# Kernel tuning notes

Hardware: AMD Instinct MI355X
Metric: run time of the kernel (lower is better)

Reference implementation:

```python
import jax, jax.numpy as jnp
import numpy as np

HEADS = 8
NUM_LANDMARKS = 256
PINV_ITERS = 6
KERNEL = 33
PAD = KERNEL // 2


def moore_penrose_iter_pinv(x, iters=PINV_ITERS):
    abs_x = jnp.abs(x)
    col = abs_x.sum(axis=-1)
    row = abs_x.sum(axis=-2)
    z = jnp.swapaxes(x, -1, -2) / (jnp.max(col) * jnp.max(row))
    I = jnp.eye(x.shape[-1], dtype=x.dtype)
    for _ in range(iters):
        xz = x @ z
        z = 0.25 * z @ (13.0 * I - xz @ (15.0 * I - xz @ (7.0 * I - xz)))
    return z


def setup_inputs() -> dict:
    key = jax.random.key(0)
    k1, k2, k3, k4 = jax.random.split(key, 4)
    b, h, n, d = 2, HEADS, 8192, 64
    q = jax.random.normal(k1, (b, h, n, d), dtype=jnp.float32)
    k = jax.random.normal(k2, (b, h, n, d), dtype=jnp.float32)
    v = jax.random.normal(k3, (b, h, n, d), dtype=jnp.float32)
    conv_w = jax.random.normal(k4, (HEADS, 1, KERNEL, 1), dtype=jnp.float32) * 0.05
    return {"q": q, "k": k, "v": v, "conv_w": conv_w}


def reference(q, k, v, conv_w):
    b, h, n, d = q.shape
    m = NUM_LANDMARKS
    l = n // m  # n chosen divisible by m, so no padding branch

    # landmarks: mean over contiguous groups of size l
    q_land = q.reshape(b, h, m, l, d).sum(axis=-2) / l  # [b,h,m,d]
    k_land = k.reshape(b, h, m, l, d).sum(axis=-2) / l

    sim1 = jnp.einsum('bhid,bhjd->bhij', q, k_land)       # [b,h,n,m]
    sim2 = jnp.einsum('bhid,bhjd->bhij', q_land, k_land)  # [b,h,m,m]
    sim3 = jnp.einsum('bhid,bhjd->bhij', q_land, k)       # [b,h,m,n]

    attn1 = jax.nn.softmax(sim1, axis=-1)
    attn2 = jax.nn.softmax(sim2, axis=-1)
    attn3 = jax.nn.softmax(sim3, axis=-1)

    attn2_inv = moore_penrose_iter_pinv(attn2, PINV_ITERS)

    out = attn1 @ (attn2_inv @ (attn3 @ v))  # [b,h,n,d]

    # depthwise residual conv over sequence dim (Conv2d(h,h,(33,1),groups=h,bias=False) on v)
    res = jax.lax.conv_general_dilated(
        v, conv_w,
        window_strides=(1, 1),
        padding=((PAD, PAD), (0, 0)),
        dimension_numbers=('NCHW', 'OIHW', 'NCHW'),
        feature_group_count=HEADS,
    )
    return out + res
```

## Files before the change

### kernel.cpp

```cpp
#include <hip/hip_runtime.h>


#define N_SEQ 8192
#define NBH   16
#define MLAND 256
#define DHEAD 64
#define NSPLIT3 8
#define MM_E  (NBH * MLAND * MLAND)
#define LM_E  (NBH * MLAND * DHEAD)

typedef __attribute__((ext_vector_type(8))) short bfrag;
typedef __attribute__((ext_vector_type(8))) _Float16 hfrag;
typedef __attribute__((ext_vector_type(4))) float f32x4;

__device__ __forceinline__ void fma8(float (&o)[8], float p, const float4& a, const float4& b) {
    o[0] += p * a.x; o[1] += p * a.y; o[2] += p * a.z; o[3] += p * a.w;
    o[4] += p * b.x; o[5] += p * b.y; o[6] += p * b.z; o[7] += p * b.w;
}

__device__ __forceinline__ float bf2f(unsigned short h) {
    return __uint_as_float(((unsigned)h) << 16);
}

__device__ __forceinline__ void splitbf(float v, unsigned short& h, unsigned short& l) {
    unsigned bits = __float_as_uint(v);
    h = (unsigned short)(bits >> 16);
    float r = v - __uint_as_float(bits & 0xffff0000u);
    l = (unsigned short)(__float_as_uint(r) >> 16);
}

__device__ __forceinline__ void splith(float v, unsigned short& h, unsigned short& l) {
    _Float16 hf = (_Float16)v;
    _Float16 lf = (_Float16)(v - (float)hf);
    h = __builtin_bit_cast(unsigned short, hf);
    l = __builtin_bit_cast(unsigned short, lf);
}

__device__ __forceinline__ void stage16(const float* __restrict__ src,
                                        unsigned short* dh, unsigned short* dl) {
    unsigned* ph = (unsigned*)dh;
    unsigned* pl = (unsigned*)dl;
    #pragma unroll
    for (int o = 0; o < 16; o += 4) {
        float4 a = *(const float4*)(src + o);
        float vv[4] = {a.x, a.y, a.z, a.w};
        unsigned short h[4], l[4];
        #pragma unroll
        for (int u = 0; u < 4; ++u) splitbf(vv[u], h[u], l[u]);
        ph[o / 2]     = (unsigned)h[0] | ((unsigned)h[1] << 16);
        ph[o / 2 + 1] = (unsigned)h[2] | ((unsigned)h[3] << 16);
        pl[o / 2]     = (unsigned)l[0] | ((unsigned)l[1] << 16);
        pl[o / 2 + 1] = (unsigned)l[2] | ((unsigned)l[3] << 16);
    }
}

__device__ __forceinline__ void stageh16(const float* __restrict__ src,
                                         unsigned short* dh, unsigned short* dl) {
    unsigned* ph = (unsigned*)dh;
    unsigned* pl = (unsigned*)dl;
    #pragma unroll
    for (int o = 0; o < 16; o += 4) {
        float4 a = *(const float4*)(src + o);
        float vv[4] = {a.x, a.y, a.z, a.w};
        unsigned short h[4], l[4];
        #pragma unroll
        for (int u = 0; u < 4; ++u) splith(vv[u], h[u], l[u]);
        ph[o / 2]     = (unsigned)h[0] | ((unsigned)h[1] << 16);
        ph[o / 2 + 1] = (unsigned)h[2] | ((unsigned)h[3] << 16);
        pl[o / 2]     = (unsigned)l[0] | ((unsigned)l[1] << 16);
        pl[o / 2 + 1] = (unsigned)l[2] | ((unsigned)l[3] << 16);
    }
}

__global__ __launch_bounds__(64) void k_landmarks(
    const float* __restrict__ q, const float* __restrict__ k,
    float* __restrict__ ql, float* __restrict__ kl)
{
    int mi = blockIdx.x & 255;
    int bh = blockIdx.x >> 8;
    const float* src = blockIdx.y ? k : q;
    float*       dst = blockIdx.y ? kl : ql;
    int t = threadIdx.x;
    const float* s = src + ((size_t)bh * N_SEQ + (size_t)mi * 32) * DHEAD;
    float acc = 0.f;
    #pragma unroll
    for (int j = 0; j < 32; ++j) acc += s[j * DHEAD + t];
    dst[((size_t)bh * MLAND + mi) * DHEAD + t] = acc * (1.f / 32.f);
}

__global__ __launch_bounds__(256) void k_sim2_softmax(
    const float* __restrict__ ql, const float* __restrict__ kl,
    unsigned short* __restrict__ xs)
{
    unsigned short* xh = xs;
    unsigned short* xl = xs + MM_E;
    int bh = blockIdx.x >> 8;
    int i  = blockIdx.x & 255;
    int t  = threadIdx.x;
    __shared__ float qrow[DHEAD];
    __shared__ float wred[8];
    if (t < DHEAD) qrow[t] = ql[((size_t)bh * MLAND + i) * DHEAD + t];
    __syncthreads();
    const float* krow = kl + ((size_t)bh * MLAND + t) * DHEAD;
    float s = 0.f;
    #pragma unroll
    for (int kk = 0; kk < DHEAD; kk += 4) {
        float4 k4 = *(const float4*)(krow + kk);
        s += qrow[kk] * k4.x + qrow[kk + 1] * k4.y + qrow[kk + 2] * k4.z + qrow[kk + 3] * k4.w;
    }
    float m = s;
    #pragma unroll
    for (int o = 32; o > 0; o >>= 1) m = fmaxf(m, __shfl_xor(m, o, 64));
    int wave = t >> 6, lane = t & 63;
    if (lane == 0) wred[wave] = m;
    __syncthreads();
    float bm = fmaxf(fmaxf(wred[0], wred[1]), fmaxf(wred[2], wred[3]));
    float e = __expf(s - bm);
    float sum = e;
    #pragma unroll
    for (int o = 32; o > 0; o >>= 1) sum += __shfl_xor(sum, o, 64);
    if (lane == 0) wred[4 + wave] = sum;
    __syncthreads();
    float bs = wred[4] + wred[5] + wred[6] + wred[7];
    float val = e / bs;
    unsigned short h, l;
    splitbf(val, h, l);
    size_t idx = ((size_t)bh * MLAND + i) * MLAND + t;
    xh[idx] = h;
    xl[idx] = l;
}

__global__ __launch_bounds__(256) void k_scale_reduce(
    const unsigned short* __restrict__ xs, float* __restrict__ scl)
{
    const unsigned short* xh = xs;
    const unsigned short* xl = xs + MM_E;
    int bh = blockIdx.x, t = threadIdx.x;
    size_t b = (size_t)bh * MLAND * MLAND;
    float colsum = 0.f, rowsum = 0.f;
    for (int i = 0; i < MLAND; ++i) {
        size_t idx = b + (size_t)i * MLAND + t;
        colsum += bf2f(xh[idx]) + bf2f(xl[idx]);
    }
    for (int j = 0; j < MLAND; ++j) {
        size_t idx = b + (size_t)t * MLAND + j;
        rowsum += bf2f(xh[idx]) + bf2f(xl[idx]);
    }
    __shared__ float red[256];
    red[t] = rowsum;
    __syncthreads();
    for (int o = 128; o > 0; o >>= 1) {
        if (t < o) red[t] = fmaxf(red[t], red[t + o]);
        __syncthreads();
    }
    if (t == 0) atomicMax((unsigned int*)&scl[0], __float_as_uint(red[0]));
    __syncthreads();
    red[t] = colsum;
    __syncthreads();
    for (int o = 128; o > 0; o >>= 1) {
        if (t < o) red[t] = fmaxf(red[t], red[t + o]);
        __syncthreads();
    }
    if (t == 0) atomicMax((unsigned int*)&scl[1], __float_as_uint(red[0]));
}

__global__ __launch_bounds__(256) void k_zinit(
    const unsigned short* __restrict__ xs, unsigned short* __restrict__ zs,
    const float* __restrict__ scl)
{
    const unsigned short* xh = xs;
    const unsigned short* xl = xs + MM_E;
    unsigned short* zh = zs;
    unsigned short* zl = zs + MM_E;
    __shared__ float tile[32][33];
    int bh = blockIdx.z;
    int i0 = blockIdx.y * 32, j0 = blockIdx.x * 32;
    int t = threadIdx.x;
    int lx = t & 31, ly = t >> 5;
    size_t b = (size_t)bh * MLAND * MLAND;
    #pragma unroll
    for (int p = 0; p < 4; ++p) {
        size_t idx = b + (size_t)(i0 + ly + 8 * p) * MLAND + j0 + lx;
        tile[ly + 8 * p][lx] = bf2f(xh[idx]) + bf2f(xl[idx]);
    }
    __syncthreads();
    float inv = 1.0f / (scl[0] * scl[1]);
    #pragma unroll
    for (int p = 0; p < 4; ++p) {
        float val = tile[lx][ly + 8 * p] * inv;
        unsigned short h, l;
        splitbf(val, h, l);
        size_t idx = b + (size_t)(j0 + ly + 8 * p) * MLAND + i0 + lx;
        zh[idx] = h;
        zl[idx] = l;
    }
}

__global__ __launch_bounds__(256) void k_bmm_planes(
    const unsigned short* __restrict__ Ahp, const unsigned short* __restrict__ Alp,
    const unsigned short* __restrict__ Bhp, const unsigned short* __restrict__ Blp,
    unsigned short* __restrict__ Chp, unsigned short* __restrict__ Clp,
    float* __restrict__ Cf,
    int N, float diag, float bscale, float outscale)
{
    __shared__ unsigned short sm[2 * 32 * 72 + 2 * 64 * 72];
    unsigned short* Ah = sm;
    unsigned short* Al = sm + 32 * 72;
    unsigned short* Bh = sm + 2 * 32 * 72;
    unsigned short* Bl = sm + 2 * 32 * 72 + 64 * 72;

    int bh = blockIdx.z;
    const size_t abase = (size_t)bh * 65536;
    const size_t bbase = (size_t)bh * 256 * N;
    int m0 = blockIdx.y * 32, n0 = blockIdx.x * 64;
    int t = threadIdx.x;
    int wave = t >> 6, lane = t & 63;
    int l15 = lane & 15, quad = lane >> 4;
    int wr = wave >> 1, wc = wave & 1;
    unsigned sflip = (bscale < 0.f) ? 0x8000u : 0u;

    f32x4 acc[2] = {};

    for (int kc = 0; kc < 256; kc += 64) {
        __syncthreads();
        {
            int m = t & 31, ks = (t >> 5) * 8;
            size_t off = abase + (size_t)(m0 + m) * 256 + kc + ks;
            *(uint4*)&Ah[m * 72 + ks] = *(const uint4*)&Ahp[off];
            *(uint4*)&Al[m * 72 + ks] = *(const uint4*)&Alp[off];
        }
        {
            int kk = t & 63, ns = (t >> 6) * 16;
            int gk = kc + kk;
            size_t off = bbase + (size_t)gk * N + n0 + ns;
            unsigned short hb[16], lb[16];
            *(uint4*)&hb[0] = *(const uint4*)&Bhp[off];
            *(uint4*)&hb[8] = *(const uint4*)&Bhp[off + 8];
            *(uint4*)&lb[0] = *(const uint4*)&Blp[off];
            *(uint4*)&lb[8] = *(const uint4*)&Blp[off + 8];
            #pragma unroll
            for (int u = 0; u < 16; ++u) {
                unsigned short h = hb[u] ^ sflip;
                unsigned short l = lb[u] ^ sflip;
                if (diag != 0.f && gk == n0 + ns + u) {
                    float val = diag + bf2f(h) + bf2f(l);
                    splitbf(val, h, l);
                }
                Bh[(ns + u) * 72 + kk] = h;
                Bl[(ns + u) * 72 + kk] = l;
            }
        }
        __syncthreads();

        #pragma unroll
        for (int k0 = 0; k0 < 64; k0 += 32) {
            int kf = k0 + quad * 8;
            int am = wr * 16 + l15;
            bfrag ah = *(const bfrag*)&Ah[am * 72 + kf];
            bfrag al = *(const bfrag*)&Al[am * 72 + kf];
            #pragma unroll
            for (int j = 0; j < 2; ++j) {
                int bn = wc * 32 + j * 16 + l15;
                bfrag bhf = *(const bfrag*)&Bh[bn * 72 + kf];
                bfrag blf = *(const bfrag*)&Bl[bn * 72 + kf];
                acc[j] = __builtin_amdgcn_mfma_f32_16x16x32_bf16(al, bhf, acc[j], 0, 0, 0);
                acc[j] = __builtin_amdgcn_mfma_f32_16x16x32_bf16(ah, blf, acc[j], 0, 0, 0);
                acc[j] = __builtin_amdgcn_mfma_f32_16x16x32_bf16(ah, bhf, acc[j], 0, 0, 0);
            }
        }
    }

    size_t cbase = (size_t)bh * 256 * N;
    if (Cf) {
        #pragma unroll
        for (int j = 0; j < 2; ++j) {
            #pragma unroll
            for (int r = 0; r < 4; ++r) {
                int row = m0 + wr * 16 + quad * 4 + r;
                int col = n0 + wc * 32 + j * 16 + l15;
                Cf[cbase + (size_t)row * N + col] = acc[j][r] * outscale;
            }
        }
    } else {
        #pragma unroll
        for (int j = 0; j < 2; ++j) {
            #pragma unroll
            for (int r = 0; r < 4; ++r) {
                int row = m0 + wr * 16 + quad * 4 + r;
                int col = n0 + wc * 32 + j * 16 + l15;
                float val = acc[j][r] * outscale;
                unsigned short h, l;
                splitbf(val, h, l);
                size_t idx = cbase + (size_t)row * N + col;
                Chp[idx] = h;
                Clp[idx] = l;
            }
        }
    }
}

__global__ __launch_bounds__(256, 2) void k_attn3_partial(
    const float* __restrict__ ql, const float* __restrict__ k,
    const float* __restrict__ v, float* __restrict__ pO,
    float* __restrict__ pm, float* __restrict__ pl)
{
    __shared__ __align__(16) unsigned short sm3[36864];
    unsigned short* QH = sm3;
    unsigned short* QL = sm3 + 4608;
    unsigned short* KH = sm3 + 9216;
    unsigned short* KL = sm3 + 13824;
    unsigned short* VH = sm3 + 18432;
    unsigned short* VL = sm3 + 23040;
    unsigned short* PH = sm3 + 27648;
    unsigned short* PL = sm3 + 32256;

    int sp = blockIdx.x;
    int m0 = blockIdx.y * 64;
    int bh = blockIdx.z;
    int t = threadIdx.x;
    int wave = t >> 6, lane = t & 63;
    int l15 = lane & 15, quad = lane >> 4;

    {
        int row = t & 63, ds = (t >> 6) * 16;
        const float* src = ql + ((size_t)bh * MLAND + m0 + row) * DHEAD + ds;
        stage16(src, &QH[row * 72 + ds], &QL[row * 72 + ds]);
    }
    __syncthreads();

    bfrag aqh[2], aql[2];
    #pragma unroll
    for (int ks = 0; ks < 2; ++ks) {
        aqh[ks] = *(const bfrag*)&QH[(wave * 16 + l15) * 72 + ks * 32 + quad * 8];
        aql[ks] = *(const bfrag*)&QL[(wave * 16 + l15) * 72 + ks * 32 + quad * 8];
    }

    f32x4 O[4] = {};
    float M[4], L[4];
    #pragma unroll
    for (int r = 0; r < 4; ++r) { M[r] = -1e30f; L[r] = 0.f; }

    const float* kb = k + (size_t)bh * N_SEQ * DHEAD;
    const float* vb = v + (size_t)bh * N_SEQ * DHEAD;

    for (int cc = 0; cc < 16; ++cc) {
        int c0 = sp * 1024 + cc * 64;
        __syncthreads();
        {
            int key = t & 63, ds = (t >> 6) * 16;
            stage16(kb + (size_t)(c0 + key) * DHEAD + ds,
                    &KH[key * 72 + ds], &KL[key * 72 + ds]);
        }
        {
            int key = t & 63, dq = (t >> 6) * 16;
            const float* src = vb + (size_t)(c0 + key) * DHEAD + dq;
            #pragma unroll
            for (int o = 0; o < 16; o += 4) {
                float4 a = *(const float4*)(src + o);
                float vv[4] = {a.x, a.y, a.z, a.w};
                #pragma unroll
                for (int u = 0; u < 4; ++u) {
                    unsigned short h, l;
                    splitbf(vv[u], h, l);
                    VH[(dq + o + u) * 72 + key] = h;
                    VL[(dq + o + u) * 72 + key] = l;
                }
            }
        }
        __syncthreads();

        f32x4 S4[4] = {};
        __builtin_amdgcn_s_setprio(1);
        #pragma unroll
        for (int ks = 0; ks < 2; ++ks) {
            #pragma unroll
            for (int ni = 0; ni < 4; ++ni) {
                bfrag bkh = *(const bfrag*)&KH[(ni * 16 + l15) * 72 + ks * 32 + quad * 8];
                bfrag bkl = *(const bfrag*)&KL[(ni * 16 + l15) * 72 + ks * 32 + quad * 8];
                S4[ni] = __builtin_amdgcn_mfma_f32_16x16x32_bf16(aql[ks], bkh, S4[ni], 0, 0, 0);
                S4[ni] = __builtin_amdgcn_mfma_f32_16x16x32_bf16(aqh[ks], bkl, S4[ni], 0, 0, 0);
                S4[ni] = __builtin_amdgcn_mfma_f32_16x16x32_bf16(aqh[ks], bkh, S4[ni], 0, 0, 0);
            }
        }
        __builtin_amdgcn_s_setprio(0);

        #pragma unroll
        for (int r = 0; r < 4; ++r) {
            float mv = fmaxf(fmaxf(S4[0][r], S4[1][r]), fmaxf(S4[2][r], S4[3][r]));
            mv = fmaxf(mv, __shfl_xor(mv, 1, 16));
            mv = fmaxf(mv, __shfl_xor(mv, 2, 16));
            mv = fmaxf(mv, __shfl_xor(mv, 4, 16));
            mv = fmaxf(mv, __shfl_xor(mv, 8, 16));
            float nM = fmaxf(M[r], mv);
            float alpha = __expf(M[r] - nM);
            M[r] = nM;
            float rs = 0.f;
            #pragma unroll
            for (int ni = 0; ni < 4; ++ni) {
                float p = __expf(S4[ni][r] - nM);
                S4[ni][r] = p;
                rs += p;
            }
            rs += __shfl_xor(rs, 1, 16);
            rs += __shfl_xor(rs, 2, 16);
            rs += __shfl_xor(rs, 4, 16);
            rs += __shfl_xor(rs, 8, 16);
            L[r] = L[r] * alpha + rs;
            #pragma unroll
            for (int ni = 0; ni < 4; ++ni) O[ni][r] *= alpha;
        }

        #pragma unroll
        for (int ni = 0; ni < 4; ++ni) {
            #pragma unroll
            for (int r = 0; r < 4; ++r) {
                int row = wave * 16 + quad * 4 + r;
                int col = ni * 16 + l15;
                unsigned short h, l;
                splitbf(S4[ni][r], h, l);
                PH[row * 72 + col] = h;
                PL[row * 72 + col] = l;
            }
        }

        __builtin_amdgcn_s_setprio(1);
        #pragma unroll
        for (int ks = 0; ks < 2; ++ks) {
            bfrag aph = *(const bfrag*)&PH[(wave * 16 + l15) * 72 + ks * 32 + quad * 8];
            bfrag apl = *(const bfrag*)&PL[(wave * 16 + l15) * 72 + ks * 32 + quad * 8];
            #pragma unroll
            for (int ni = 0; ni < 4; ++ni) {
                bfrag bvh = *(const bfrag*)&VH[(ni * 16 + l15) * 72 + ks * 32 + quad * 8];
                bfrag bvl = *(const bfrag*)&VL[(ni * 16 + l15) * 72 + ks * 32 + quad * 8];
                O[ni] = __builtin_amdgcn_mfma_f32_16x16x32_bf16(apl, bvh, O[ni], 0, 0, 0);
                O[ni] = __builtin_amdgcn_mfma_f32_16x16x32_bf16(aph, bvl, O[ni], 0, 0, 0);
                O[ni] = __builtin_amdgcn_mfma_f32_16x16x32_bf16(aph, bvh, O[ni], 0, 0, 0);
            }
        }
        __builtin_amdgcn_s_setprio(0);
    }

    int base = (bh * NSPLIT3 + sp) * MLAND + m0;
    #pragma unroll
    for (int r = 0; r < 4; ++r) {
        int row = wave * 16 + quad * 4 + r;
        if (l15 == 0) { pm[base + row] = M[r]; pl[base + row] = L[r]; }
        #pragma unroll
        for (int ni = 0; ni < 4; ++ni)
            pO[(size_t)(base + row) * DHEAD + ni * 16 + l15] = O[ni][r];
    }
}

__global__ __launch_bounds__(64) void k_attn3_combine(
    const float* __restrict__ pO, const float* __restrict__ pm,
    const float* __restrict__ pl, unsigned short* __restrict__ kvs)
{
    unsigned short* kvh = kvs;
    unsigned short* kvl = kvs + LM_E;
    int bh = blockIdx.x >> 8;
    int m  = blockIdx.x & 255;
    int d  = threadIdx.x;
    float M = -1e30f;
    #pragma unroll
    for (int s = 0; s < NSPLIT3; ++s) M = fmaxf(M, pm[(bh * NSPLIT3 + s) * MLAND + m]);
    float L = 0.f, O = 0.f;
    #pragma unroll
    for (int s = 0; s < NSPLIT3; ++s) {
        int base = (bh * NSPLIT3 + s) * MLAND + m;
        float w = __expf(pm[base] - M);
        L += pl[base] * w;
        O += w * pO[(size_t)base * DHEAD + d];
    }
    float val = O / L;
    unsigned short h, l;
    splitbf(val, h, l);
    size_t idx = ((size_t)bh * MLAND + m) * DHEAD + d;
    kvh[idx] = h;
    kvl[idx] = l;
}

__global__ __launch_bounds__(256, 2) void k_attn1_mfma(
    const float* __restrict__ q, const float* __restrict__ kl,
    const float* __restrict__ W, float* __restrict__ out)
{
    __shared__ __align__(16) unsigned short sm1[36864];
    unsigned short* QH = sm1;
    unsigned short* QL = sm1 + 4608;
    unsigned short* KH = sm1 + 9216;
    unsigned short* KL = sm1 + 13824;
    unsigned short* WH = sm1 + 18432;
    unsigned short* WL = sm1 + 23040;
    unsigned short* PH = sm1 + 27648;
    unsigned short* PL = sm1 + 32256;

    int bh = blockIdx.y;
    int r0 = blockIdx.x * 64;
    int t = threadIdx.x;
    int wave = t >> 6, lane = t & 63;
    int l15 = lane & 15, quad = lane >> 4;

    {
        int row = t & 63, ds = (t >> 6) * 16;
        const float* src = q + ((size_t)bh * N_SEQ + r0 + row) * DHEAD + ds;
        stageh16(src, &QH[row * 72 + ds], &QL[row * 72 + ds]);
    }
    __syncthreads();

    hfrag aqh[2], aql[2];
    #pragma unroll
    for (int ks = 0; ks < 2; ++ks) {
        aqh[ks] = *(const hfrag*)&QH[(wave * 16 + l15) * 72 + ks * 32 + quad * 8];
        aql[ks] = *(const hfrag*)&QL[(wave * 16 + l15) * 72 + ks * 32 + quad * 8];
    }

    f32x4 O4[4] = {};
    float M[4], L[4];
    #pragma unroll
    for (int r = 0; r < 4; ++r) { M[r] = -1e30f; L[r] = 0.f; }

    for (int mc = 0; mc < 4; ++mc) {
        __syncthreads();
        {
            int key = t & 63, ds = (t >> 6) * 16;
            stageh16(kl + ((size_t)bh * MLAND + mc * 64 + key) * DHEAD + ds,
                     &KH[key * 72 + ds], &KL[key * 72 + ds]);
        }
        {
            int key = t & 63, dq = (t >> 6) * 16;
            const float* src = W + ((size_t)bh * MLAND + mc * 64 + key) * DHEAD + dq;
            #pragma unroll
            for (int o = 0; o < 16; o += 4) {
                float4 a = *(const float4*)(src + o);
                float vv[4] = {a.x * 0.015625f, a.y * 0.015625f,
                               a.z * 0.015625f, a.w * 0.015625f};
                #pragma unroll
                for (int u = 0; u < 4; ++u) {
                    unsigned short h, l;
                    splith(vv[u], h, l);
                    WH[(dq + o + u) * 72 + key] = h;
                    WL[(dq + o + u) * 72 + key] = l;
                }
            }
        }
        __syncthreads();

        f32x4 S4[4] = {};
        __builtin_amdgcn_s_setprio(1);
        #pragma unroll
        for (int ks = 0; ks < 2; ++ks) {
            #pragma unroll
            for (int ni = 0; ni < 4; ++ni) {
                hfrag bkh = *(const hfrag*)&KH[(ni * 16 + l15) * 72 + ks * 32 + quad * 8];
                hfrag bkl = *(const hfrag*)&KL[(ni * 16 + l15) * 72 + ks * 32 + quad * 8];
                S4[ni] = __builtin_amdgcn_mfma_f32_16x16x32_f16(aql[ks], bkh, S4[ni], 0, 0, 0);
                S4[ni] = __builtin_amdgcn_mfma_f32_16x16x32_f16(aqh[ks], bkl, S4[ni], 0, 0, 0);
                S4[ni] = __builtin_amdgcn_mfma_f32_16x16x32_f16(aqh[ks], bkh, S4[ni], 0, 0, 0);
            }
        }
        __builtin_amdgcn_s_setprio(0);

        #pragma unroll
        for (int r = 0; r < 4; ++r) {
            float mv = fmaxf(fmaxf(S4[0][r], S4[1][r]), fmaxf(S4[2][r], S4[3][r]));
            mv = fmaxf(mv, __shfl_xor(mv, 1, 16));
            mv = fmaxf(mv, __shfl_xor(mv, 2, 16));
            mv = fmaxf(mv, __shfl_xor(mv, 4, 16));
            mv = fmaxf(mv, __shfl_xor(mv, 8, 16));
            float nM = fmaxf(M[r], mv);
            float alpha = __expf(M[r] - nM);
            M[r] = nM;
            float rs = 0.f;
            #pragma unroll
            for (int ni = 0; ni < 4; ++ni) {
                float p = __expf(S4[ni][r] - nM);
                S4[ni][r] = p;
                rs += p;
            }
            rs += __shfl_xor(rs, 1, 16);
            rs += __shfl_xor(rs, 2, 16);
            rs += __shfl_xor(rs, 4, 16);
            rs += __shfl_xor(rs, 8, 16);
            L[r] = L[r] * alpha + rs;
            #pragma unroll
            for (int ni = 0; ni < 4; ++ni) O4[ni][r] *= alpha;
        }

        #pragma unroll
        for (int ni = 0; ni < 4; ++ni) {
            #pragma unroll
            for (int r = 0; r < 4; ++r) {
                int row = wave * 16 + quad * 4 + r;
                int col = ni * 16 + l15;
                unsigned short h, l;
                splith(S4[ni][r], h, l);
                PH[row * 72 + col] = h;
                PL[row * 72 + col] = l;
            }
        }

        __builtin_amdgcn_s_setprio(1);
        #pragma unroll
        for (int ks = 0; ks < 2; ++ks) {
            hfrag aph = *(const hfrag*)&PH[(wave * 16 + l15) * 72 + ks * 32 + quad * 8];
            hfrag apl = *(const hfrag*)&PL[(wave * 16 + l15) * 72 + ks * 32 + quad * 8];
            #pragma unroll
            for (int ni = 0; ni < 4; ++ni) {
                hfrag bwh = *(const hfrag*)&WH[(ni * 16 + l15) * 72 + ks * 32 + quad * 8];
                hfrag bwl = *(const hfrag*)&WL[(ni * 16 + l15) * 72 + ks * 32 + quad * 8];
                O4[ni] = __builtin_amdgcn_mfma_f32_16x16x32_f16(apl, bwh, O4[ni], 0, 0, 0);
                O4[ni] = __builtin_amdgcn_mfma_f32_16x16x32_f16(aph, bwl, O4[ni], 0, 0, 0);
                O4[ni] = __builtin_amdgcn_mfma_f32_16x16x32_f16(aph, bwh, O4[ni], 0, 0, 0);
            }
        }
        __builtin_amdgcn_s_setprio(0);
    }

    float inv[4];
    #pragma unroll
    for (int r = 0; r < 4; ++r) inv[r] = 64.0f / L[r];
    #pragma unroll
    for (int r = 0; r < 4; ++r) {
        int row = wave * 16 + quad * 4 + r;
        float* dst = out + ((size_t)bh * N_SEQ + r0 + row) * DHEAD;
        #pragma unroll
        for (int ni = 0; ni < 4; ++ni)
            dst[ni * 16 + l15] = O4[ni][r] * inv[r];
    }
}

__global__ __launch_bounds__(256) void k_conv_add(
    const float* __restrict__ v, const float* __restrict__ cw,
    float* __restrict__ out)
{
    __shared__ __align__(16) float smem[160 * 68];
    __shared__ float wgt[33];
    int bh = blockIdx.y;
    int r0 = blockIdx.x * 128;
    int t = threadIdx.x;
    int wave = t >> 6, lane = t & 63;
    int ly = lane >> 3, lx = lane & 7;
    int rb = wave * 32 + ly * 4;

    if (t < 33) wgt[t] = cw[(bh & 7) * 33 + t];

    for (int rr = t; rr < 160; rr += 256) {
        int gr = r0 - 16 + rr;
        bool ok = (gr >= 0) && (gr < N_SEQ);
        const float* src = v + ((size_t)bh * N_SEQ + gr) * DHEAD;
        #pragma unroll
        for (int c = 0; c < 64; c += 4) {
            float4 val = ok ? *(const float4*)(src + c) : make_float4(0.f, 0.f, 0.f, 0.f);
            *(float4*)&smem[rr * 68 + c] = val;
        }
    }
    __syncthreads();

    float res[4][8] = {};
    #pragma unroll
    for (int w = 0; w < 36; ++w) {
        float4 va  = *(const float4*)&smem[(rb + w) * 68 + lx * 8];
        float4 vb4 = *(const float4*)&smem[(rb + w) * 68 + lx * 8 + 4];
        #pragma unroll
        for (int i = 0; i < 4; ++i) {
            if (w - i >= 0 && w - i <= 32) {
                float wv = wgt[w - i];
                fma8(res[i], wv, va, vb4);
            }
        }
    }

    #pragma unroll
    for (int i = 0; i < 4; ++i) {
        float* dst = out + ((size_t)bh * N_SEQ + r0 + rb + i) * DHEAD + lx * 8;
        float4 o0 = *(const float4*)dst;
        float4 o1 = *(const float4*)(dst + 4);
        *(float4*)dst = make_float4(o0.x + res[i][0], o0.y + res[i][1],
                                    o0.z + res[i][2], o0.w + res[i][3]);
        *(float4*)(dst + 4) = make_float4(o1.x + res[i][4], o1.y + res[i][5],
                                          o1.z + res[i][6], o1.w + res[i][7]);
    }
}

extern "C" void kernel_launch(void* const* d_in, const int* in_sizes, int n_in,
                              void* d_out, int out_size, void* d_ws, size_t ws_size,
                              hipStream_t stream)
{
    (void)in_sizes; (void)n_in; (void)out_size; (void)ws_size;
    const float* q  = (const float*)d_in[0];
    const float* k  = (const float*)d_in[1];
    const float* v  = (const float*)d_in[2];
    const float* cw = (const float*)d_in[3];
    float* out = (float*)d_out;
    float* ws  = (float*)d_ws;

    const size_t LM = (size_t)LM_E;
    const size_t MM = (size_t)MM_E;

    float* ql  = ws;
    float* kl  = ql  + LM;
    float* xsf = kl  + LM;
    float* zsf = xsf + MM;
    float* big = zsf + MM;
    float* kvf = big + 4 * MM;
    float* W   = kvf + LM;
    float* scl = W   + LM;
    float* pm  = scl + 16;
    float* pl  = pm + (size_t)NBH * NSPLIT3 * MLAND;

    float* pO = big;

    unsigned short* xs  = (unsigned short*)xsf;
    unsigned short* zs  = (unsigned short*)zsf;
    unsigned short* bgu = (unsigned short*)big;
    unsigned short* kvs = (unsigned short*)kvf;

    unsigned short* xh  = xs;
    unsigned short* xl  = xs + MM;
    unsigned short* zh  = zs;
    unsigned short* zl  = zs + MM;
    unsigned short* z2h = bgu;
    unsigned short* z2l = bgu + MM;
    unsigned short* xzh = bgu + 2 * MM;
    unsigned short* xzl = bgu + 3 * MM;
    unsigned short* t2h = bgu + 4 * MM;
    unsigned short* t2l = bgu + 5 * MM;
    unsigned short* t3h = bgu + 6 * MM;
    unsigned short* t3l = bgu + 7 * MM;
    unsigned short* kvh = kvs;
    unsigned short* kvl = kvs + LM;

    hipMemsetAsync(scl, 0, 32, stream);

    k_landmarks<<<dim3(NBH * MLAND, 2), 64, 0, stream>>>(q, k, ql, kl);
    k_sim2_softmax<<<NBH * MLAND, 256, 0, stream>>>(ql, kl, xs);
    k_scale_reduce<<<NBH, 256, 0, stream>>>(xs, scl);
    k_zinit<<<dim3(8, 8, NBH), 256, 0, stream>>>(xs, zs, scl);

    k_attn3_partial<<<dim3(NSPLIT3, 4, NBH), 256, 0, stream>>>(ql, k, v, pO, pm, pl);
    k_attn3_combine<<<NBH * MLAND, 64, 0, stream>>>(pO, pm, pl, kvs);

    unsigned short *zch = zh, *zcl = zl, *znh = z2h, *znl = z2l;
    for (int it = 0; it < 6; ++it) {
        k_bmm_planes<<<dim3(4, 8, NBH), 256, 0, stream>>>(
            xh, xl, zch, zcl, xzh, xzl, nullptr, 256, 0.f, 1.f, 1.f);
        k_bmm_planes<<<dim3(4, 8, NBH), 256, 0, stream>>>(
            xzh, xzl, xzh, xzl, t2h, t2l, nullptr, 256, 7.f, -1.f, 1.f);
        k_bmm_planes<<<dim3(4, 8, NBH), 256, 0, stream>>>(
            xzh, xzl, t2h, t2l, t3h, t3l, nullptr, 256, 15.f, -1.f, 1.f);
        k_bmm_planes<<<dim3(4, 8, NBH), 256, 0, stream>>>(
            zch, zcl, t3h, t3l, znh, znl, nullptr, 256, 13.f, -1.f, 0.25f);
        unsigned short* th = zch; zch = znh; znh = th;
        unsigned short* tl = zcl; zcl = znl; znl = tl;
    }
    k_bmm_planes<<<dim3(1, 8, NBH), 256, 0, stream>>>(
        zch, zcl, kvh, kvl, nullptr, nullptr, W, 64, 0.f, 1.f, 1.f);

    k_attn1_mfma<<<dim3(128, NBH), 256, 0, stream>>>(q, kl, W, out);
    k_conv_add<<<dim3(64, NBH), 256, 0, stream>>>(v, cw, out);
}
```

Measured before the change: 600.6 us.

## Split scale reduction across more blocks and remap bmm blocks per XCD

The scale reduction kernel now runs 16 blocks per head instead of one. Each block computes partial row and column sums over a 16-row or 16-column segment, then combines them with shuffles and shared memory before the atomic max. This is meant to remove the long serial loops of the single-block version. The batched matmul kernel now uses a 1-D grid whose block index is decoded so that blocks landing on the same XCD share a head's matrices, aiming for better L2 locality. The XCD remapping assumes round-robin block dispatch across 8 XCDs.

Result: faster. 568.1 us (-5.4%).

```diff
diff --git a/kernel.cpp b/kernel.cpp
--- a/kernel.cpp
+++ b/kernel.cpp
@@ -135,33 +135,60 @@
 {
     const unsigned short* xh = xs;
     const unsigned short* xl = xs + MM_E;
-    int bh = blockIdx.x, t = threadIdx.x;
+    int bh = blockIdx.y, seg = blockIdx.x;
+    int t = threadIdx.x;
     size_t b = (size_t)bh * MLAND * MLAND;
-    float colsum = 0.f, rowsum = 0.f;
-    for (int i = 0; i < MLAND; ++i) {
-        size_t idx = b + (size_t)i * MLAND + t;
-        colsum += bf2f(xh[idx]) + bf2f(xl[idx]);
-    }
-    for (int j = 0; j < MLAND; ++j) {
-        size_t idx = b + (size_t)t * MLAND + j;
-        rowsum += bf2f(xh[idx]) + bf2f(xl[idx]);
-    }
-    __shared__ float red[256];
-    red[t] = rowsum;
-    __syncthreads();
-    for (int o = 128; o > 0; o >>= 1) {
-        if (t < o) red[t] = fmaxf(red[t], red[t + o]);
-        __syncthreads();
-    }
-    if (t == 0) atomicMax((unsigned int*)&scl[0], __float_as_uint(red[0]));
-    __syncthreads();
-    red[t] = colsum;
-    __syncthreads();
-    for (int o = 128; o > 0; o >>= 1) {
-        if (t < o) red[t] = fmaxf(red[t], red[t + o]);
-        __syncthreads();
-    }
-    if (t == 0) atomicMax((unsigned int*)&scl[1], __float_as_uint(red[0]));
+    __shared__ float red[32];
+    __shared__ float red2[256];
+
+    {
+        int r = seg * 16 + (t >> 4);
+        int j0 = (t & 15) * 16;
+        float rp = 0.f;
+        #pragma unroll
+        for (int j = 0; j < 16; ++j) {
+            size_t idx = b + (size_t)r * MLAND + j0 + j;
+            rp += bf2f(xh[idx]) + bf2f(xl[idx]);
+        }
+        rp += __shfl_xor(rp, 1, 16);
+        rp += __shfl_xor(rp, 2, 16);
+        rp += __shfl_xor(rp, 4, 16);
+        rp += __shfl_xor(rp, 8, 16);
+        if ((t & 15) == 0) red[t >> 4] = rp;
+        __syncthreads();
+        if (t == 0) {
+            float m = red[0];
+            #pragma unroll
+            for (int i = 1; i < 16; ++i) m = fmaxf(m, red[i]);
+            atomicMax((unsigned int*)&scl[0], __float_as_uint(m));
+        }
+        __syncthreads();
+    }
+    {
+        int c = seg * 16 + (t & 15);
+        int i0 = (t >> 4) * 16;
+        float cp = 0.f;
+        #pragma unroll
+        for (int i = 0; i < 16; ++i) {
+            size_t idx = b + (size_t)(i0 + i) * MLAND + c;
+            cp += bf2f(xh[idx]) + bf2f(xl[idx]);
+        }
+        red2[t] = cp;
+        __syncthreads();
+        if (t < 16) {
+            float s = 0.f;
+            #pragma unroll
+            for (int g = 0; g < 16; ++g) s += red2[g * 16 + t];
+            red[t] = s;
+        }
+        __syncthreads();
+        if (t == 0) {
+            float m = red[0];
+            #pragma unroll
+            for (int i = 1; i < 16; ++i) m = fmaxf(m, red[i]);
+            atomicMax((unsigned int*)&scl[1], __float_as_uint(m));
+        }
+    }
 }
 
 __global__ __launch_bounds__(256) void k_zinit(
@@ -209,10 +236,16 @@
     unsigned short* Bh = sm + 2 * 32 * 72;
     unsigned short* Bl = sm + 2 * 32 * 72 + 64 * 72;
 
-    int bh = blockIdx.z;
+    int ntn = N >> 6;
+    int bid = blockIdx.x;
+    int xcd  = bid & 7;
+    int slot = bid >> 3;
+    int bh   = xcd + 8 * (slot & 1);
+    int tile = slot >> 1;
+    int m0 = (tile / ntn) * 32, n0 = (tile % ntn) * 64;
+
     const size_t abase = (size_t)bh * 65536;
     const size_t bbase = (size_t)bh * 256 * N;
-    int m0 = blockIdx.y * 32, n0 = blockIdx.x * 64;
     int t = threadIdx.x;
     int wave = t >> 6, lane = t & 63;
     int l15 = lane & 15, quad = lane >> 4;
@@ -733,7 +766,7 @@
 
     k_landmarks<<<dim3(NBH * MLAND, 2), 64, 0, stream>>>(q, k, ql, kl);
     k_sim2_softmax<<<NBH * MLAND, 256, 0, stream>>>(ql, kl, xs);
-    k_scale_reduce<<<NBH, 256, 0, stream>>>(xs, scl);
+    k_scale_reduce<<<dim3(16, NBH), 256, 0, stream>>>(xs, scl);
     k_zinit<<<dim3(8, 8, NBH), 256, 0, stream>>>(xs, zs, scl);
 
     k_attn3_partial<<<dim3(NSPLIT3, 4, NBH), 256, 0, stream>>>(ql, k, v, pO, pm, pl);
@@ -741,18 +774,18 @@
 
     unsigned short *zch = zh, *zcl = zl, *znh = z2h, *znl = z2l;
     for (int it = 0; it < 6; ++it) {
-        k_bmm_planes<<<dim3(4, 8, NBH), 256, 0, stream>>>(
+        k_bmm_planes<<<512, 256, 0, stream>>>(
             xh, xl, zch, zcl, xzh, xzl, nullptr, 256, 0.f, 1.f, 1.f);
-        k_bmm_planes<<<dim3(4, 8, NBH), 256, 0, stream>>>(
+        k_bmm_planes<<<512, 256, 0, stream>>>(
             xzh, xzl, xzh, xzl, t2h, t2l, nullptr, 256, 7.f, -1.f, 1.f);
-        k_bmm_planes<<<dim3(4, 8, NBH), 256, 0, stream>>>(
+        k_bmm_planes<<<512, 256, 0, stream>>>(
             xzh, xzl, t2h, t2l, t3h, t3l, nullptr, 256, 15.f, -1.f, 1.f);
-        k_bmm_planes<<<dim3(4, 8, NBH), 256, 0, stream>>>(
+        k_bmm_planes<<<512, 256, 0, stream>>>(
             zch, zcl, t3h, t3l, znh, znl, nullptr, 256, 13.f, -1.f, 0.25f);
         unsigned short* th = zch; zch = znh; znh = th;
         unsigned short* tl = zcl; zcl = znl; znl = tl;
     }
-    k_bmm_planes<<<dim3(1, 8, NBH), 256, 0, stream>>>(
+    k_bmm_planes<<<128, 256, 0, stream>>>(
         zch, zcl, kvh, kvl, nullptr, nullptr, W, 64, 0.f, 1.f, 1.f);
 
     k_attn1_mfma<<<dim3(128, NBH), 256, 0, stream>>>(q, kl, W, out);
```
